# Optimization experiments

Hardware: AMD Instinct MI355X
Metric: run time of the kernel (lower is better)

Reference implementation:

```python
import jax, jax.numpy as jnp
import numpy as np

# Model config (matches init_kwargs)
L_F, DELTA_F, L_S, DELTA_S = 1, 1, 32, 16
HIDDEN = 32       # SSM state dim H
GRU_H = 64        # slow-branch GRU hidden
N_GRU = 4
B, T = 4, 32768


def setup_inputs() -> dict:
    key = jax.random.key(0)
    ks = jax.random.split(key, 13)
    def nrm(k, shape, s=0.05):
        return jax.random.normal(k, shape, dtype=jnp.float32) * s
    return {
        "x": jax.random.normal(ks[0], (B, T), dtype=jnp.float32),
        # SlowBranch params
        "fc_in_w": nrm(ks[1], (GRU_H, 1), 0.3),
        "fc_in_b": nrm(ks[2], (GRU_H,)),
        "gru_wih": nrm(ks[3], (N_GRU, 3 * GRU_H, GRU_H), 0.1),
        "gru_whh": nrm(ks[4], (N_GRU, 3 * GRU_H, GRU_H), 0.1),
        "gru_bih": nrm(ks[5], (N_GRU, 3 * GRU_H)),
        "gru_bhh": nrm(ks[6], (N_GRU, 3 * GRU_H)),
        "out_fc_w": nrm(ks[7], (2 * HIDDEN, GRU_H), 0.1),
        "out_fc_b": nrm(ks[8], (2 * HIDDEN,)),
        # Fast branch params (F_IN: 1->H, F_OUT: H->1)
        "fin_w": nrm(ks[9], (HIDDEN, 1), 0.3),
        "fin_b": nrm(ks[10], (HIDDEN,)),
        "fout_w": nrm(ks[11], (1, HIDDEN), 0.1),
        "fout_b": nrm(ks[12], (1,)),
    }


def _gru_layer(xs, Wih, Whh, bih, bhh):
    """Torch-convention GRU layer. xs: (N, L, H_in) -> (N, L, H)."""
    H = Whh.shape[1]
    # Precompute input-side gate pre-activations: (N, L, 3H)
    xp = jnp.einsum('nlh,gh->nlg', xs, Wih) + bih
    def step(h, xt):
        gh = h @ Whh.T + bhh                       # (N, 3H)
        ir, iz, inew = jnp.split(xt, 3, axis=-1)
        hr, hz, hnew = jnp.split(gh, 3, axis=-1)
        r = jax.nn.sigmoid(ir + hr)
        z = jax.nn.sigmoid(iz + hz)
        n = jnp.tanh(inew + r * hnew)
        h = (1.0 - z) * n + z * h
        return h, h
    h0 = jnp.zeros((xs.shape[0], H), xs.dtype)
    _, ys = jax.lax.scan(step, h0, jnp.swapaxes(xp, 0, 1))  # (L, N, H)
    return jnp.swapaxes(ys, 0, 1)


def reference(x, fc_in_w, fc_in_b, gru_wih, gru_whh, gru_bih, gru_bhh,
              out_fc_w, out_fc_b, fin_w, fin_b, fout_w, fout_b):
    Bsz, Tlen = x.shape
    num_slow = (Tlen - L_S) // DELTA_S + 1

    frame_idx = jnp.arange(num_slow)[:, None] * DELTA_S + jnp.arange(L_S)[None, :]
    x_s = x[:, frame_idx].reshape(Bsz * num_slow, L_S, 1)      # (N, L_s, 1)
    h = jax.nn.relu(x_s * fc_in_w[:, 0] + fc_in_b)             # (N, L_s, GRU_H)
    for l in range(gru_wih.shape[0]):
        h = _gru_layer(h, gru_wih[l], gru_whh[l], gru_bih[l], gru_bhh[l])
    eps = h[:, -1, :] @ out_fc_w.T + out_fc_b                  # (N, 2H)
    eps = eps.reshape(Bsz, num_slow, 2 * HIDDEN)
    A_slow = jax.nn.sigmoid(eps[..., :HIDDEN])                 # (B, S, H)
    g_slow = eps[..., HIDDEN:]                                 # (B, S, H)

    # ---- Fast branch: per-sample diagonal linear SSM scan ----
    delta = DELTA_S // DELTA_F
    idx = jnp.clip(jnp.arange(Tlen) // delta - 1, 0, num_slow - 1)  # (T,)
    A_t = A_slow[:, idx, :]                                    # (B, T, H)
    u_t = (x[..., None] * fin_w[:, 0] + fin_b) * g_slow[:, idx, :]  # (B, T, H)

    def step(hc, inp):
        A, u = inp
        hn = A * hc + u
        return hn, hn
    h0 = jnp.zeros((Bsz, HIDDEN), x.dtype)
    _, h_all = jax.lax.scan(step, h0,
                            (jnp.swapaxes(A_t, 0, 1), jnp.swapaxes(u_t, 0, 1)))
    # h_all: (T, B, H); F_OUT applied to every state
    return jnp.einsum('tbh,h->bt', h_all, fout_w[0]) + fout_b[0]   # (B, T)
```

## Files before the change

### kernel.cpp

```cpp
#include <hip/hip_runtime.h>
#include <hip/hip_bf16.h>

typedef __bf16 bf16x8 __attribute__((ext_vector_type(8)));
typedef short short8 __attribute__((ext_vector_type(8)));
typedef float f32x4 __attribute__((ext_vector_type(4)));
typedef unsigned short ushort_t;

#define T_LEN 32768
#define B_SZ 4
#define NSLOW 2047
#define NSEQ (B_SZ * NSLOW)
#define GH 64
#define G3 192
#define NL 4
#define HID 32
#define NCH 256
#define L2E 1.44269504088896341f

#define OFF_X    0
#define OFF_FCW  131072
#define OFF_FCB  131136
#define OFF_WIH  131200
#define OFF_WHH  180352
#define OFF_BIH  229504
#define OFF_BHH  230272
#define OFF_OFW  231040
#define OFF_OFB  235136
#define OFF_FINW 235200
#define OFF_FINB 235232
#define OFF_FOW  235264
#define OFF_FOB  235296
#define CONV_TOTAL 235297
#define CONV_PAD_BYTES 470656

static __device__ __forceinline__ float bf2f(ushort_t u) {
    union { unsigned u; float f; } c; c.u = ((unsigned)u) << 16; return c.f;
}
static __device__ __forceinline__ ushort_t f2bf(float f) {
    union { float f; unsigned u; } c; c.f = f;
    unsigned r = (c.u + 0x7FFFu + ((c.u >> 16) & 1u)) >> 16;
    return (ushort_t)r;
}
static __device__ __forceinline__ unsigned pk2bf(float a, float b) {
    float2 f; f.x = a; f.y = b;
    __hip_bfloat162 h = __float22bfloat162_rn(f);
    unsigned u;
    __builtin_memcpy(&u, &h, 4);
    return u;
}
static __device__ __forceinline__ f32x4 mfma16(short8 a, short8 b, f32x4 c) {
    return __builtin_amdgcn_mfma_f32_16x16x32_bf16(
        __builtin_bit_cast(bf16x8, a), __builtin_bit_cast(bf16x8, b), c, 0, 0, 0);
}
static __device__ __forceinline__ int xoff(int t, int kb, int seq) {
    return ((((t << 3) + kb) << 4) + (seq ^ (kb & 7))) << 3;
}
static __device__ __forceinline__ short8 load_frag_scaled(const ushort_t* p, float s) {
    uint4 r = *(const uint4*)p;
    unsigned aa[4] = {r.x, r.y, r.z, r.w};
    short8 o;
#pragma unroll
    for (int i = 0; i < 4; ++i) {
        o[2 * i]     = (short)f2bf(bf2f((ushort_t)(aa[i] & 0xffffu)) * s);
        o[2 * i + 1] = (short)f2bf(bf2f((ushort_t)(aa[i] >> 16)) * s);
    }
    return o;
}

struct Ptrs13 { const void* p[13]; };

__global__ __launch_bounds__(256) void convert_kernel(Ptrs13 ptrs,
                                                      int* __restrict__ flag,
                                                      ushort_t* __restrict__ dst)
{
    __shared__ int scnt;
    if (threadIdx.x == 0) scnt = 0;
    __syncthreads();
    {
        ushort_t u = ((const ushort_t*)ptrs.p[0])[threadIdx.x];
        int e = (u >> 7) & 0xFF;
        int ok = (e >= 80 && e <= 141) ? 1 : 0;
#pragma unroll
        for (int d = 1; d < 64; d <<= 1) ok += __shfl_xor(ok, d, 64);
        if ((threadIdx.x & 63) == 0) atomicAdd(&scnt, ok);
    }
    __syncthreads();
    const bool isbf = (scnt >= 224);
    if (blockIdx.x == 0 && threadIdx.x == 0) *flag = isbf ? 1 : 0;

    const int offs[14] = {OFF_X, OFF_FCW, OFF_FCB, OFF_WIH, OFF_WHH, OFF_BIH,
                          OFF_BHH, OFF_OFW, OFF_OFB, OFF_FINW, OFF_FINB,
                          OFF_FOW, OFF_FOB, CONV_TOTAL};
    for (int idx = blockIdx.x * 256 + threadIdx.x; idx < CONV_TOTAL;
         idx += gridDim.x * 256) {
        int s = 0;
#pragma unroll
        for (int j = 1; j < 13; ++j) if (idx >= offs[j]) s = j;
        int k = idx - offs[s];
        ushort_t v = isbf ? ((const ushort_t*)ptrs.p[s])[k]
                          : f2bf(((const float*)ptrs.p[s])[k]);
        dst[idx] = v;
    }
}

__global__ __launch_bounds__(256, 2) void gru_kernel(
    const ushort_t* __restrict__ x, const ushort_t* __restrict__ fcw,
    const ushort_t* __restrict__ fcb, const ushort_t* __restrict__ wih,
    const ushort_t* __restrict__ whh, const ushort_t* __restrict__ bih,
    const ushort_t* __restrict__ bhh, const ushort_t* __restrict__ ofw,
    const ushort_t* __restrict__ ofb, float* __restrict__ Aslow,
    float* __restrict__ gslow)
{
    __shared__ short8 Xs8[4096];
    short* Xs = (short*)Xs8;
    const int tid = threadIdx.x;
    const int w = tid >> 6, lane = tid & 63;
    const int q = lane >> 4, m = lane & 15;
    const int jb = w * 16;
    const int n0 = blockIdx.x * 16;

#pragma unroll 1
    for (int ii = 0; ii < 16; ++ii) {
        int cid = ii * 256 + tid;
        int seq = cid & 15, kb = (cid >> 4) & 7, t = cid >> 7;
        int n = n0 + seq; if (n > NSEQ - 1) n = NSEQ - 1;
        int b = n / NSLOW, s = n - b * NSLOW;
        float xv = bf2f(x[b * T_LEN + s * 16 + t]);
        short8 v;
#pragma unroll
        for (int i = 0; i < 8; ++i) {
            int g = kb * 8 + i;
            float h = fmaf(xv, bf2f(fcw[g]), bf2f(fcb[g]));
            h = h > 0.f ? h : 0.f;
            v[i] = (short)f2bf(h);
        }
        Xs8[xoff(t, kb, seq) >> 3] = v;
    }

    const int col0 = jb + 4 * q;
    const int kbw = (col0 >> 3);
    const int wsub = (col0 & 7);
    const int kofs = q * 8;
    const int wbase0 = ((kbw << 4) + (m ^ (kbw & 7))) * 8 + wsub;

    float hc[4];
#pragma unroll 1
    for (int l = 0; l < NL; ++l) {
        const ushort_t* wl = wih + l * G3 * GH;
        const ushort_t* ul = whh + l * G3 * GH;
        short8 wR0 = load_frag_scaled(wl + (0 * 64 + jb + m) * 64 + kofs, -L2E);
        short8 wR1 = load_frag_scaled(wl + (0 * 64 + jb + m) * 64 + 32 + kofs, -L2E);
        short8 wZ0 = load_frag_scaled(wl + (1 * 64 + jb + m) * 64 + kofs, -L2E);
        short8 wZ1 = load_frag_scaled(wl + (1 * 64 + jb + m) * 64 + 32 + kofs, -L2E);
        short8 wN0 = load_frag_scaled(wl + (2 * 64 + jb + m) * 64 + kofs, 2.f * L2E);
        short8 wN1 = load_frag_scaled(wl + (2 * 64 + jb + m) * 64 + 32 + kofs, 2.f * L2E);
        short8 uR0 = load_frag_scaled(ul + (0 * 64 + jb + m) * 64 + kofs, -L2E);
        short8 uR1 = load_frag_scaled(ul + (0 * 64 + jb + m) * 64 + 32 + kofs, -L2E);
        short8 uZ0 = load_frag_scaled(ul + (1 * 64 + jb + m) * 64 + kofs, -L2E);
        short8 uZ1 = load_frag_scaled(ul + (1 * 64 + jb + m) * 64 + 32 + kofs, -L2E);
        short8 uN0 = load_frag_scaled(ul + (2 * 64 + jb + m) * 64 + kofs, 2.f * L2E);
        short8 uN1 = load_frag_scaled(ul + (2 * 64 + jb + m) * 64 + 32 + kofs, 2.f * L2E);

        f32x4 bRv, bZv, bNXv, bNHv;
#pragma unroll
        for (int i = 0; i < 4; ++i) {
            int c = col0 + i;
            bRv[i]  = -L2E * (bf2f(bih[l * G3 + c]) + bf2f(bhh[l * G3 + c]));
            bZv[i]  = -L2E * (bf2f(bih[l * G3 + 64 + c]) + bf2f(bhh[l * G3 + 64 + c]));
            bNXv[i] = 2.f * L2E * bf2f(bih[l * G3 + 128 + c]);
            bNHv[i] = 2.f * L2E * bf2f(bhh[l * G3 + 128 + c]);
        }

        hc[0] = hc[1] = hc[2] = hc[3] = 0.f;

        __syncthreads();
        int iA = xoff(0, q, m) >> 3;
        int iB = xoff(0, 4 + q, m) >> 3;
        int wb = wbase0;

        short8 cx0 = Xs8[iA], cx1 = Xs8[iB];
        short8 nx0 = Xs8[iA + 128], nx1 = Xs8[iB + 128];
        f32x4 xR = bRv, xZ = bZv, xN = bNXv;
        xR = mfma16(wR0, cx0, xR); xR = mfma16(wR1, cx1, xR);
        xZ = mfma16(wZ0, cx0, xZ); xZ = mfma16(wZ1, cx1, xZ);
        xN = mfma16(wN0, cx0, xN); xN = mfma16(wN1, cx1, xN);
#pragma unroll
        for (int i = 0; i < 4; ++i) {
            float r = __builtin_amdgcn_rcpf(1.f + __builtin_amdgcn_exp2f(xR[i]));
            float z = __builtin_amdgcn_rcpf(1.f + __builtin_amdgcn_exp2f(xZ[i]));
            float yp = fmaf(r, bNHv[i], xN[i]);
            float nn = fmaf(-2.f,
                __builtin_amdgcn_rcpf(1.f + __builtin_amdgcn_exp2f(yp)), 1.f);
            hc[i] = fmaf(z, hc[i] - nn, nn);
        }
        *(uint2*)(Xs + wb) = make_uint2(pk2bf(hc[0], hc[1]), pk2bf(hc[2], hc[3]));
        xR = bRv; xZ = bZv; xN = bNXv;
        xR = mfma16(wR0, nx0, xR); xR = mfma16(wR1, nx1, xR);
        xZ = mfma16(wZ0, nx0, xZ); xZ = mfma16(wZ1, nx1, xZ);
        xN = mfma16(wN0, nx0, xN); xN = mfma16(wN1, nx1, xN);
        iA += 128; iB += 128; wb += 1024;

#pragma unroll 1
        for (int t = 1; t < 32; ++t) {
            __syncthreads();
            short8 bh0 = Xs8[iA - 128];
            short8 bh1 = Xs8[iB - 128];
            short8 px0, px1;
            if (t < 31) {
                px0 = Xs8[iA + 128];
                px1 = Xs8[iB + 128];
            }
            f32x4 aR = xR, aZ = xZ, aNH = bNHv;
            aR  = mfma16(uR0, bh0, aR);  aR  = mfma16(uR1, bh1, aR);
            aZ  = mfma16(uZ0, bh0, aZ);  aZ  = mfma16(uZ1, bh1, aZ);
            aNH = mfma16(uN0, bh0, aNH); aNH = mfma16(uN1, bh1, aNH);
#pragma unroll
            for (int i = 0; i < 4; ++i) {
                float r = __builtin_amdgcn_rcpf(1.f + __builtin_amdgcn_exp2f(aR[i]));
                float z = __builtin_amdgcn_rcpf(1.f + __builtin_amdgcn_exp2f(aZ[i]));
                float yp = fmaf(r, aNH[i], xN[i]);
                float nn = fmaf(-2.f,
                    __builtin_amdgcn_rcpf(1.f + __builtin_amdgcn_exp2f(yp)), 1.f);
                hc[i] = fmaf(z, hc[i] - nn, nn);
            }
            *(uint2*)(Xs + wb) =
                make_uint2(pk2bf(hc[0], hc[1]), pk2bf(hc[2], hc[3]));
            if (t < 31) {
                xR = bRv; xZ = bZv; xN = bNXv;
                xR = mfma16(wR0, px0, xR); xR = mfma16(wR1, px1, xR);
                xZ = mfma16(wZ0, px0, xZ); xZ = mfma16(wZ1, px1, xZ);
                xN = mfma16(wN0, px0, xN); xN = mfma16(wN1, px1, xN);
            }
            iA += 128; iB += 128; wb += 1024;
        }
    }

    __syncthreads();
    short8 aL0 = Xs8[xoff(31, q, m) >> 3];
    short8 aL1 = Xs8[xoff(31, 4 + q, m) >> 3];
    float sc = (w < 2) ? -L2E : 1.f;
    short8 o0 = load_frag_scaled(ofw + (jb + m) * 64 + kofs, sc);
    short8 o1 = load_frag_scaled(ofw + (jb + m) * 64 + 32 + kofs, sc);
    f32x4 aE = {bf2f(ofb[col0]) * sc, bf2f(ofb[col0 + 1]) * sc,
                bf2f(ofb[col0 + 2]) * sc, bf2f(ofb[col0 + 3]) * sc};
    aE = mfma16(o0, aL0, aE);
    aE = mfma16(o1, aL1, aE);
    int n = n0 + m;
    if (w < 2) {
        f32x4 v;
#pragma unroll
        for (int i = 0; i < 4; ++i)
            v[i] = __builtin_amdgcn_rcpf(1.f + __builtin_amdgcn_exp2f(aE[i]));
        *(f32x4*)(Aslow + n * HID + col0) = v;
    } else {
        *(f32x4*)(gslow + n * HID + (col0 - 32)) = aE;
    }
}

__global__ __launch_bounds__(256) void pass1_kernel(
    const ushort_t* __restrict__ x, const float* __restrict__ Aslow,
    const float* __restrict__ gslow, const ushort_t* __restrict__ finw,
    const ushort_t* __restrict__ finb, float* __restrict__ P,
    float* __restrict__ S)
{
    int gt = blockIdx.x * 256 + threadIdx.x;
    int h = gt & 31, c = (gt >> 5) & 255, b = gt >> 13;
    float fw = bf2f(finw[h]), fb = bf2f(finb[h]);
    float Pv = 1.f, Sv = 0.f;
    int t0 = c * 128;
#pragma unroll 1
    for (int seg = 0; seg < 8; ++seg) {
        int sidx = (t0 >> 4) + seg - 1;
        if (sidx < 0) sidx = 0;
        if (sidx > NSLOW - 1) sidx = NSLOW - 1;
        float A = Aslow[(b * NSLOW + sidx) * HID + h];
        float g = gslow[(b * NSLOW + sidx) * HID + h];
        float fwg = fw * g, fbg = fb * g;
        const uint4* px = (const uint4*)(x + b * T_LEN + t0 + seg * 16);
        uint4 ra = px[0], rb = px[1];
        unsigned xa[8] = {ra.x, ra.y, ra.z, ra.w, rb.x, rb.y, rb.z, rb.w};
#pragma unroll
        for (int j = 0; j < 8; ++j) {
            float x0 = bf2f((ushort_t)(xa[j] & 0xffffu));
            float x1 = bf2f((ushort_t)(xa[j] >> 16));
            Sv = fmaf(A, Sv, fmaf(x0, fwg, fbg));
            Sv = fmaf(A, Sv, fmaf(x1, fwg, fbg));
        }
        float A2 = A * A, A4 = A2 * A2, A8 = A4 * A4;
        Pv *= A8 * A8;
    }
    P[(b * HID + h) * NCH + c] = Pv;
    S[(b * HID + h) * NCH + c] = Sv;
}

__global__ __launch_bounds__(128) void scan_kernel(
    const float* __restrict__ P, const float* __restrict__ S,
    float* __restrict__ Hpre)
{
    int tid = threadIdx.x;
    const float4* p4 = (const float4*)(P + tid * NCH);
    const float4* s4 = (const float4*)(S + tid * NCH);
    float* hp = Hpre + tid * NCH;
    float hr = 0.f;
#pragma unroll 8
    for (int c = 0; c < NCH / 4; ++c) {
        float4 pv = p4[c], sv = s4[c];
        hp[4 * c + 0] = hr; hr = fmaf(pv.x, hr, sv.x);
        hp[4 * c + 1] = hr; hr = fmaf(pv.y, hr, sv.y);
        hp[4 * c + 2] = hr; hr = fmaf(pv.z, hr, sv.z);
        hp[4 * c + 3] = hr; hr = fmaf(pv.w, hr, sv.w);
    }
}

__global__ __launch_bounds__(256) void pass2_kernel(
    const ushort_t* __restrict__ x, const float* __restrict__ Aslow,
    const float* __restrict__ gslow, const float* __restrict__ Hpre,
    const ushort_t* __restrict__ finw, const ushort_t* __restrict__ finb,
    const ushort_t* __restrict__ fow, const ushort_t* __restrict__ fob,
    const int* __restrict__ flag, void* __restrict__ outv)
{
    int wv = blockIdx.x * 4 + (threadIdx.x >> 6);
    int lane = threadIdx.x & 63;
    int half = lane >> 5, h = lane & 31;
    int pair = wv * 2 + half;
    int b = pair >> 8, c = pair & 255;
    const bool isbf = (*flag != 0);
    ushort_t* outb = (ushort_t*)outv;
    float* outf = (float*)outv;
    float hv = Hpre[(b * HID + h) * NCH + c];
    float fw = bf2f(finw[h]), fb = bf2f(finb[h]);
    float wo = bf2f(fow[h]), ob = bf2f(fob[0]);
    int t0 = c * 128;
#pragma unroll 1
    for (int blk = 0; blk < 4; ++blk) {
        float ykeep = 0.f;
        float A = 0.f, fwg = 0.f, fbg = 0.f;
#pragma unroll
        for (int tt = 0; tt < 32; ++tt) {
            int t = t0 + blk * 32 + tt;
            if ((tt & 15) == 0) {
                int sidx = (t >> 4) - 1;
                if (sidx < 0) sidx = 0;
                A = Aslow[(b * NSLOW + sidx) * HID + h];
                float g = gslow[(b * NSLOW + sidx) * HID + h];
                fwg = fw * g; fbg = fb * g;
            }
            float xv = bf2f(x[b * T_LEN + t]);
            hv = fmaf(A, hv, fmaf(xv, fwg, fbg));
            float y = hv * wo;
            y += __shfl_xor(y, 1, 64);
            y += __shfl_xor(y, 2, 64);
            y += __shfl_xor(y, 4, 64);
            y += __shfl_xor(y, 8, 64);
            y += __shfl_xor(y, 16, 64);
            if (tt == h) ykeep = y + ob;
        }
        int oidx = b * T_LEN + t0 + blk * 32 + h;
        if (isbf) outb[oidx] = f2bf(ykeep);
        else      outf[oidx] = ykeep;
    }
}

extern "C" void kernel_launch(void* const* d_in, const int* in_sizes, int n_in,
                              void* d_out, int out_size, void* d_ws, size_t ws_size,
                              hipStream_t stream)
{
    ushort_t* cv = (ushort_t*)d_ws;
    const ushort_t* x    = cv + OFF_X;
    const ushort_t* fcw  = cv + OFF_FCW;
    const ushort_t* fcb  = cv + OFF_FCB;
    const ushort_t* wih  = cv + OFF_WIH;
    const ushort_t* whh  = cv + OFF_WHH;
    const ushort_t* bih  = cv + OFF_BIH;
    const ushort_t* bhh  = cv + OFF_BHH;
    const ushort_t* ofw  = cv + OFF_OFW;
    const ushort_t* ofb  = cv + OFF_OFB;
    const ushort_t* finw = cv + OFF_FINW;
    const ushort_t* finb = cv + OFF_FINB;
    const ushort_t* fow  = cv + OFF_FOW;
    const ushort_t* fob  = cv + OFF_FOB;

    float* Aslow = (float*)((char*)d_ws + CONV_PAD_BYTES);
    float* gslow = Aslow + 8192 * 32;
    float* P     = gslow + 8192 * 32;
    float* S     = P + 4 * 32 * NCH;
    float* Hpre  = S + 4 * 32 * NCH;
    int*   flag  = (int*)(Hpre + 4 * 32 * NCH);

    Ptrs13 ptrs;
    for (int i = 0; i < 13; ++i) ptrs.p[i] = d_in[i];

    convert_kernel<<<dim3(920), dim3(256), 0, stream>>>(ptrs, flag, cv);
    gru_kernel<<<dim3(512), dim3(256), 0, stream>>>(
        x, fcw, fcb, wih, whh, bih, bhh, ofw, ofb, Aslow, gslow);
    pass1_kernel<<<dim3(128), dim3(256), 0, stream>>>(
        x, Aslow, gslow, finw, finb, P, S);
    scan_kernel<<<dim3(1), dim3(128), 0, stream>>>(P, S, Hpre);
    pass2_kernel<<<dim3(128), dim3(256), 0, stream>>>(
        x, Aslow, gslow, Hpre, finw, finb, fow, fob, flag, d_out);
}
```

Baseline: 193.1 us.

## Pipeline pairs of GRU layers in a staggered wavefront over timesteps

The GRU layers now run two at a time: layer 2p+1 trails layer 2p by two timesteps, and both share the in-place LDS sequence buffer within one loop. This replaces 64 barrier-separated serial steps per layer pair with 34, and lets the independent MFMA and transcendental chains of the two layers overlap to hide recurrence latency. Per-layer weights and state move into a struct, so two full sets of weight fragments stay live at once. That roughly doubles register pressure and risks spills under the 2-blocks-per-SM launch bound. Correctness depends on the two-step skew keeping the in-place reads and writes from overlapping.

Measured after the change: 198.3 us. 2.7% more time.

```diff
diff --git a/kernel.cpp b/kernel.cpp
--- a/kernel.cpp
+++ b/kernel.cpp
@@ -103,6 +103,93 @@
     }
 }
 
+struct LayerState {
+    short8 wR0, wR1, wZ0, wZ1, wN0, wN1;
+    short8 uR0, uR1, uZ0, uZ1, uN0, uN1;
+    f32x4 bR, bZ, bNX, bNH;
+    f32x4 xR, xZ, xN;
+    f32x4 hc;
+};
+
+static __device__ __forceinline__ void load_layer(
+    LayerState& L, int l, const ushort_t* __restrict__ wih,
+    const ushort_t* __restrict__ whh, const ushort_t* __restrict__ bih,
+    const ushort_t* __restrict__ bhh, int jb, int m, int kofs, int col0)
+{
+    const ushort_t* wl = wih + l * G3 * GH;
+    const ushort_t* ul = whh + l * G3 * GH;
+    L.wR0 = load_frag_scaled(wl + (0 * 64 + jb + m) * 64 + kofs, -L2E);
+    L.wR1 = load_frag_scaled(wl + (0 * 64 + jb + m) * 64 + 32 + kofs, -L2E);
+    L.wZ0 = load_frag_scaled(wl + (1 * 64 + jb + m) * 64 + kofs, -L2E);
+    L.wZ1 = load_frag_scaled(wl + (1 * 64 + jb + m) * 64 + 32 + kofs, -L2E);
+    L.wN0 = load_frag_scaled(wl + (2 * 64 + jb + m) * 64 + kofs, 2.f * L2E);
+    L.wN1 = load_frag_scaled(wl + (2 * 64 + jb + m) * 64 + 32 + kofs, 2.f * L2E);
+    L.uR0 = load_frag_scaled(ul + (0 * 64 + jb + m) * 64 + kofs, -L2E);
+    L.uR1 = load_frag_scaled(ul + (0 * 64 + jb + m) * 64 + 32 + kofs, -L2E);
+    L.uZ0 = load_frag_scaled(ul + (1 * 64 + jb + m) * 64 + kofs, -L2E);
+    L.uZ1 = load_frag_scaled(ul + (1 * 64 + jb + m) * 64 + 32 + kofs, -L2E);
+    L.uN0 = load_frag_scaled(ul + (2 * 64 + jb + m) * 64 + kofs, 2.f * L2E);
+    L.uN1 = load_frag_scaled(ul + (2 * 64 + jb + m) * 64 + 32 + kofs, 2.f * L2E);
+#pragma unroll
+    for (int i = 0; i < 4; ++i) {
+        int c = col0 + i;
+        L.bR[i]  = -L2E * (bf2f(bih[l * G3 + c]) + bf2f(bhh[l * G3 + c]));
+        L.bZ[i]  = -L2E * (bf2f(bih[l * G3 + 64 + c]) + bf2f(bhh[l * G3 + 64 + c]));
+        L.bNX[i] = 2.f * L2E * bf2f(bih[l * G3 + 128 + c]);
+        L.bNH[i] = 2.f * L2E * bf2f(bhh[l * G3 + 128 + c]);
+    }
+    L.hc[0] = L.hc[1] = L.hc[2] = L.hc[3] = 0.f;
+}
+
+static __device__ __forceinline__ void gru_step(
+    LayerState& L, int t, short8* Xs8, short* Xs, int iA0, int iB0, int wb0)
+{
+    if (t < 0 || t > 31) return;
+    const int iA = iA0 + (t << 7);
+    const int iB = iB0 + (t << 7);
+    short8 px0, px1;
+    if (t < 31) {
+        px0 = Xs8[iA + 128];
+        px1 = Xs8[iB + 128];
+    }
+    f32x4 aR, aZ, aNH = L.bNH;
+    if (t == 0) {
+        short8 cx0 = Xs8[iA], cx1 = Xs8[iB];
+        f32x4 xR = L.bR, xZ = L.bZ, xN = L.bNX;
+        xR = mfma16(L.wR0, cx0, xR); xR = mfma16(L.wR1, cx1, xR);
+        xZ = mfma16(L.wZ0, cx0, xZ); xZ = mfma16(L.wZ1, cx1, xZ);
+        xN = mfma16(L.wN0, cx0, xN); xN = mfma16(L.wN1, cx1, xN);
+        L.xR = xR; L.xZ = xZ; L.xN = xN;
+        aR = xR; aZ = xZ;
+    } else {
+        short8 bh0 = Xs8[iA - 128];
+        short8 bh1 = Xs8[iB - 128];
+        aR  = mfma16(L.uR0, bh0, L.xR); aR  = mfma16(L.uR1, bh1, aR);
+        aZ  = mfma16(L.uZ0, bh0, L.xZ); aZ  = mfma16(L.uZ1, bh1, aZ);
+        aNH = mfma16(L.uN0, bh0, aNH);  aNH = mfma16(L.uN1, bh1, aNH);
+    }
+    f32x4 hcv = L.hc;
+#pragma unroll
+    for (int i = 0; i < 4; ++i) {
+        float r = __builtin_amdgcn_rcpf(1.f + __builtin_amdgcn_exp2f(aR[i]));
+        float z = __builtin_amdgcn_rcpf(1.f + __builtin_amdgcn_exp2f(aZ[i]));
+        float yp = fmaf(r, aNH[i], L.xN[i]);
+        float nn = fmaf(-2.f,
+            __builtin_amdgcn_rcpf(1.f + __builtin_amdgcn_exp2f(yp)), 1.f);
+        hcv[i] = fmaf(z, hcv[i] - nn, nn);
+    }
+    L.hc = hcv;
+    *(uint2*)(Xs + wb0 + (t << 10)) =
+        make_uint2(pk2bf(hcv[0], hcv[1]), pk2bf(hcv[2], hcv[3]));
+    if (t < 31) {
+        f32x4 xR = L.bR, xZ = L.bZ, xN = L.bNX;
+        xR = mfma16(L.wR0, px0, xR); xR = mfma16(L.wR1, px1, xR);
+        xZ = mfma16(L.wZ0, px0, xZ); xZ = mfma16(L.wZ1, px1, xZ);
+        xN = mfma16(L.wN0, px0, xN); xN = mfma16(L.wN1, px1, xN);
+        L.xR = xR; L.xZ = xZ; L.xN = xN;
+    }
+}
+
 __global__ __launch_bounds__(256, 2) void gru_kernel(
     const ushort_t* __restrict__ x, const ushort_t* __restrict__ fcw,
     const ushort_t* __restrict__ fcb, const ushort_t* __restrict__ wih,
@@ -142,96 +229,19 @@
     const int wsub = (col0 & 7);
     const int kofs = q * 8;
     const int wbase0 = ((kbw << 4) + (m ^ (kbw & 7))) * 8 + wsub;
-
-    float hc[4];
+    const int iA0 = xoff(0, q, m) >> 3;
+    const int iB0 = xoff(0, 4 + q, m) >> 3;
+
 #pragma unroll 1
-    for (int l = 0; l < NL; ++l) {
-        const ushort_t* wl = wih + l * G3 * GH;
-        const ushort_t* ul = whh + l * G3 * GH;
-        short8 wR0 = load_frag_scaled(wl + (0 * 64 + jb + m) * 64 + kofs, -L2E);
-        short8 wR1 = load_frag_scaled(wl + (0 * 64 + jb + m) * 64 + 32 + kofs, -L2E);
-        short8 wZ0 = load_frag_scaled(wl + (1 * 64 + jb + m) * 64 + kofs, -L2E);
-        short8 wZ1 = load_frag_scaled(wl + (1 * 64 + jb + m) * 64 + 32 + kofs, -L2E);
-        short8 wN0 = load_frag_scaled(wl + (2 * 64 + jb + m) * 64 + kofs, 2.f * L2E);
-        short8 wN1 = load_frag_scaled(wl + (2 * 64 + jb + m) * 64 + 32 + kofs, 2.f * L2E);
-        short8 uR0 = load_frag_scaled(ul + (0 * 64 + jb + m) * 64 + kofs, -L2E);
-        short8 uR1 = load_frag_scaled(ul + (0 * 64 + jb + m) * 64 + 32 + kofs, -L2E);
-        short8 uZ0 = load_frag_scaled(ul + (1 * 64 + jb + m) * 64 + kofs, -L2E);
-        short8 uZ1 = load_frag_scaled(ul + (1 * 64 + jb + m) * 64 + 32 + kofs, -L2E);
-        short8 uN0 = load_frag_scaled(ul + (2 * 64 + jb + m) * 64 + kofs, 2.f * L2E);
-        short8 uN1 = load_frag_scaled(ul + (2 * 64 + jb + m) * 64 + 32 + kofs, 2.f * L2E);
-
-        f32x4 bRv, bZv, bNXv, bNHv;
-#pragma unroll
-        for (int i = 0; i < 4; ++i) {
-            int c = col0 + i;
-            bRv[i]  = -L2E * (bf2f(bih[l * G3 + c]) + bf2f(bhh[l * G3 + c]));
-            bZv[i]  = -L2E * (bf2f(bih[l * G3 + 64 + c]) + bf2f(bhh[l * G3 + 64 + c]));
-            bNXv[i] = 2.f * L2E * bf2f(bih[l * G3 + 128 + c]);
-            bNHv[i] = 2.f * L2E * bf2f(bhh[l * G3 + 128 + c]);
-        }
-
-        hc[0] = hc[1] = hc[2] = hc[3] = 0.f;
-
-        __syncthreads();
-        int iA = xoff(0, q, m) >> 3;
-        int iB = xoff(0, 4 + q, m) >> 3;
-        int wb = wbase0;
-
-        short8 cx0 = Xs8[iA], cx1 = Xs8[iB];
-        short8 nx0 = Xs8[iA + 128], nx1 = Xs8[iB + 128];
-        f32x4 xR = bRv, xZ = bZv, xN = bNXv;
-        xR = mfma16(wR0, cx0, xR); xR = mfma16(wR1, cx1, xR);
-        xZ = mfma16(wZ0, cx0, xZ); xZ = mfma16(wZ1, cx1, xZ);
-        xN = mfma16(wN0, cx0, xN); xN = mfma16(wN1, cx1, xN);
-#pragma unroll
-        for (int i = 0; i < 4; ++i) {
-            float r = __builtin_amdgcn_rcpf(1.f + __builtin_amdgcn_exp2f(xR[i]));
-            float z = __builtin_amdgcn_rcpf(1.f + __builtin_amdgcn_exp2f(xZ[i]));
-            float yp = fmaf(r, bNHv[i], xN[i]);
-            float nn = fmaf(-2.f,
-                __builtin_amdgcn_rcpf(1.f + __builtin_amdgcn_exp2f(yp)), 1.f);
-            hc[i] = fmaf(z, hc[i] - nn, nn);
-        }
-        *(uint2*)(Xs + wb) = make_uint2(pk2bf(hc[0], hc[1]), pk2bf(hc[2], hc[3]));
-        xR = bRv; xZ = bZv; xN = bNXv;
-        xR = mfma16(wR0, nx0, xR); xR = mfma16(wR1, nx1, xR);
-        xZ = mfma16(wZ0, nx0, xZ); xZ = mfma16(wZ1, nx1, xZ);
-        xN = mfma16(wN0, nx0, xN); xN = mfma16(wN1, nx1, xN);
-        iA += 128; iB += 128; wb += 1024;
-
+    for (int p = 0; p < 2; ++p) {
+        LayerState LA, LB;
+        load_layer(LA, 2 * p,     wih, whh, bih, bhh, jb, m, kofs, col0);
+        load_layer(LB, 2 * p + 1, wih, whh, bih, bhh, jb, m, kofs, col0);
 #pragma unroll 1
-        for (int t = 1; t < 32; ++t) {
+        for (int s = 0; s < 34; ++s) {
             __syncthreads();
-            short8 bh0 = Xs8[iA - 128];
-            short8 bh1 = Xs8[iB - 128];
-            short8 px0, px1;
-            if (t < 31) {
-                px0 = Xs8[iA + 128];
-                px1 = Xs8[iB + 128];
-            }
-            f32x4 aR = xR, aZ = xZ, aNH = bNHv;
-            aR  = mfma16(uR0, bh0, aR);  aR  = mfma16(uR1, bh1, aR);
-            aZ  = mfma16(uZ0, bh0, aZ);  aZ  = mfma16(uZ1, bh1, aZ);
-            aNH = mfma16(uN0, bh0, aNH); aNH = mfma16(uN1, bh1, aNH);
-#pragma unroll
-            for (int i = 0; i < 4; ++i) {
-                float r = __builtin_amdgcn_rcpf(1.f + __builtin_amdgcn_exp2f(aR[i]));
-                float z = __builtin_amdgcn_rcpf(1.f + __builtin_amdgcn_exp2f(aZ[i]));
-                float yp = fmaf(r, aNH[i], xN[i]);
-                float nn = fmaf(-2.f,
-                    __builtin_amdgcn_rcpf(1.f + __builtin_amdgcn_exp2f(yp)), 1.f);
-                hc[i] = fmaf(z, hc[i] - nn, nn);
-            }
-            *(uint2*)(Xs + wb) =
-                make_uint2(pk2bf(hc[0], hc[1]), pk2bf(hc[2], hc[3]));
-            if (t < 31) {
-                xR = bRv; xZ = bZv; xN = bNXv;
-                xR = mfma16(wR0, px0, xR); xR = mfma16(wR1, px1, xR);
-                xZ = mfma16(wZ0, px0, xZ); xZ = mfma16(wZ1, px1, xZ);
-                xN = mfma16(wN0, px0, xN); xN = mfma16(wN1, px1, xN);
-            }
-            iA += 128; iB += 128; wb += 1024;
+            gru_step(LA, s,     Xs8, Xs, iA0, iB0, wbase0);
+            gru_step(LB, s - 2, Xs8, Xs, iA0, iB0, wbase0);
         }
     }
 
```

## Wavefront-pipeline the four GRU layers across warp groups with a shared-memory ring

Applied to the files above, without the earlier changes.

The GRU kernel grows from 256 to 1024 threads per block so that each group of four waves owns one GRU layer. The layers run as a diagonal wavefront: layer l handles timestep s-2l and hands its hidden states to the next layer through a 4-slot ring buffer in LDS. This replaces the serial layer-by-layer loop, cutting the number of barrier-separated steps per block from 128 to 38 and keeping each layer's weights resident in registers. In exchange every block needs much more LDS and many more threads, and the 1024-thread launch bound may squeeze registers and lower occupancy.

Result: slower. 203.6 us (+5.4%).

```diff
diff --git a/kernel.cpp b/kernel.cpp
--- a/kernel.cpp
+++ b/kernel.cpp
@@ -103,7 +103,7 @@
     }
 }
 
-__global__ __launch_bounds__(256, 2) void gru_kernel(
+__global__ __launch_bounds__(1024, 4) void gru_kernel(
     const ushort_t* __restrict__ x, const ushort_t* __restrict__ fcw,
     const ushort_t* __restrict__ fcb, const ushort_t* __restrict__ wih,
     const ushort_t* __restrict__ whh, const ushort_t* __restrict__ bih,
@@ -111,17 +111,19 @@
     const ushort_t* __restrict__ ofb, float* __restrict__ Aslow,
     float* __restrict__ gslow)
 {
-    __shared__ short8 Xs8[4096];
-    short* Xs = (short*)Xs8;
+    __shared__ short8 X0s[4096];
+    __shared__ short8 Rg[2048];
+    short* RgS = (short*)Rg;
     const int tid = threadIdx.x;
-    const int w = tid >> 6, lane = tid & 63;
+    const int W = tid >> 6, lane = tid & 63;
+    const int l = W >> 2, w = W & 3;
     const int q = lane >> 4, m = lane & 15;
     const int jb = w * 16;
     const int n0 = blockIdx.x * 16;
 
 #pragma unroll 1
-    for (int ii = 0; ii < 16; ++ii) {
-        int cid = ii * 256 + tid;
+    for (int ii = 0; ii < 4; ++ii) {
+        int cid = ii * 1024 + tid;
         int seq = cid & 15, kb = (cid >> 4) & 7, t = cid >> 7;
         int n = n0 + seq; if (n > NSEQ - 1) n = NSEQ - 1;
         int b = n / NSLOW, s = n - b * NSLOW;
@@ -134,7 +136,7 @@
             h = h > 0.f ? h : 0.f;
             v[i] = (short)f2bf(h);
         }
-        Xs8[xoff(t, kb, seq) >> 3] = v;
+        X0s[xoff(t, kb, seq) >> 3] = v;
     }
 
     const int col0 = jb + 4 * q;
@@ -142,118 +144,104 @@
     const int wsub = (col0 & 7);
     const int kofs = q * 8;
     const int wbase0 = ((kbw << 4) + (m ^ (kbw & 7))) * 8 + wsub;
-
-    float hc[4];
+    const int iA0 = (q << 4) + (m ^ q);
+    const int iB0 = ((4 + q) << 4) + (m ^ ((4 + q) & 7));
+
+    const ushort_t* wl = wih + l * G3 * GH;
+    const ushort_t* ul = whh + l * G3 * GH;
+    short8 wR0 = load_frag_scaled(wl + (0 * 64 + jb + m) * 64 + kofs, -L2E);
+    short8 wR1 = load_frag_scaled(wl + (0 * 64 + jb + m) * 64 + 32 + kofs, -L2E);
+    short8 wZ0 = load_frag_scaled(wl + (1 * 64 + jb + m) * 64 + kofs, -L2E);
+    short8 wZ1 = load_frag_scaled(wl + (1 * 64 + jb + m) * 64 + 32 + kofs, -L2E);
+    short8 wN0 = load_frag_scaled(wl + (2 * 64 + jb + m) * 64 + kofs, 2.f * L2E);
+    short8 wN1 = load_frag_scaled(wl + (2 * 64 + jb + m) * 64 + 32 + kofs, 2.f * L2E);
+    short8 uR0 = load_frag_scaled(ul + (0 * 64 + jb + m) * 64 + kofs, -L2E);
+    short8 uR1 = load_frag_scaled(ul + (0 * 64 + jb + m) * 64 + 32 + kofs, -L2E);
+    short8 uZ0 = load_frag_scaled(ul + (1 * 64 + jb + m) * 64 + kofs, -L2E);
+    short8 uZ1 = load_frag_scaled(ul + (1 * 64 + jb + m) * 64 + 32 + kofs, -L2E);
+    short8 uN0 = load_frag_scaled(ul + (2 * 64 + jb + m) * 64 + kofs, 2.f * L2E);
+    short8 uN1 = load_frag_scaled(ul + (2 * 64 + jb + m) * 64 + 32 + kofs, 2.f * L2E);
+
+    f32x4 bRv, bZv, bNXv, bNHv;
+#pragma unroll
+    for (int i = 0; i < 4; ++i) {
+        int c = col0 + i;
+        bRv[i]  = -L2E * (bf2f(bih[l * G3 + c]) + bf2f(bhh[l * G3 + c]));
+        bZv[i]  = -L2E * (bf2f(bih[l * G3 + 64 + c]) + bf2f(bhh[l * G3 + 64 + c]));
+        bNXv[i] = 2.f * L2E * bf2f(bih[l * G3 + 128 + c]);
+        bNHv[i] = 2.f * L2E * bf2f(bhh[l * G3 + 128 + c]);
+    }
+
+    const short8* inb = (l == 0) ? X0s : (Rg + (l - 1) * 512);
+    const short8* ringL = Rg + l * 512;
+    const int wbL = l * 4096 + wbase0;
+
+    float hc[4] = {0.f, 0.f, 0.f, 0.f};
+    f32x4 xR = {0.f, 0.f, 0.f, 0.f}, xZ = xR, xN = xR;
+
 #pragma unroll 1
-    for (int l = 0; l < NL; ++l) {
-        const ushort_t* wl = wih + l * G3 * GH;
-        const ushort_t* ul = whh + l * G3 * GH;
-        short8 wR0 = load_frag_scaled(wl + (0 * 64 + jb + m) * 64 + kofs, -L2E);
-        short8 wR1 = load_frag_scaled(wl + (0 * 64 + jb + m) * 64 + 32 + kofs, -L2E);
-        short8 wZ0 = load_frag_scaled(wl + (1 * 64 + jb + m) * 64 + kofs, -L2E);
-        short8 wZ1 = load_frag_scaled(wl + (1 * 64 + jb + m) * 64 + 32 + kofs, -L2E);
-        short8 wN0 = load_frag_scaled(wl + (2 * 64 + jb + m) * 64 + kofs, 2.f * L2E);
-        short8 wN1 = load_frag_scaled(wl + (2 * 64 + jb + m) * 64 + 32 + kofs, 2.f * L2E);
-        short8 uR0 = load_frag_scaled(ul + (0 * 64 + jb + m) * 64 + kofs, -L2E);
-        short8 uR1 = load_frag_scaled(ul + (0 * 64 + jb + m) * 64 + 32 + kofs, -L2E);
-        short8 uZ0 = load_frag_scaled(ul + (1 * 64 + jb + m) * 64 + kofs, -L2E);
-        short8 uZ1 = load_frag_scaled(ul + (1 * 64 + jb + m) * 64 + 32 + kofs, -L2E);
-        short8 uN0 = load_frag_scaled(ul + (2 * 64 + jb + m) * 64 + kofs, 2.f * L2E);
-        short8 uN1 = load_frag_scaled(ul + (2 * 64 + jb + m) * 64 + 32 + kofs, 2.f * L2E);
-
-        f32x4 bRv, bZv, bNXv, bNHv;
+    for (int s = 0; s < 38; ++s) {
+        __syncthreads();
+        int t = s - 2 * l;
+        if ((unsigned)t > 31u) continue;
+
+        f32x4 aR, aZ, aNH = bNHv;
+        if (t == 0) {
+            short8 cx0 = inb[iA0], cx1 = inb[iB0];
+            xR = bRv; xZ = bZv; xN = bNXv;
+            xR = mfma16(wR0, cx0, xR); xR = mfma16(wR1, cx1, xR);
+            xZ = mfma16(wZ0, cx0, xZ); xZ = mfma16(wZ1, cx1, xZ);
+            xN = mfma16(wN0, cx0, xN); xN = mfma16(wN1, cx1, xN);
+            aR = xR; aZ = xZ;
+        } else {
+            int si = ((t - 1) & 3) << 7;
+            short8 bh0 = ringL[si + iA0], bh1 = ringL[si + iB0];
+            aR  = mfma16(uR0, bh0, xR);  aR  = mfma16(uR1, bh1, aR);
+            aZ  = mfma16(uZ0, bh0, xZ);  aZ  = mfma16(uZ1, bh1, aZ);
+            aNH = mfma16(uN0, bh0, aNH); aNH = mfma16(uN1, bh1, aNH);
+        }
 #pragma unroll
         for (int i = 0; i < 4; ++i) {
-            int c = col0 + i;
-            bRv[i]  = -L2E * (bf2f(bih[l * G3 + c]) + bf2f(bhh[l * G3 + c]));
-            bZv[i]  = -L2E * (bf2f(bih[l * G3 + 64 + c]) + bf2f(bhh[l * G3 + 64 + c]));
-            bNXv[i] = 2.f * L2E * bf2f(bih[l * G3 + 128 + c]);
-            bNHv[i] = 2.f * L2E * bf2f(bhh[l * G3 + 128 + c]);
-        }
-
-        hc[0] = hc[1] = hc[2] = hc[3] = 0.f;
-
-        __syncthreads();
-        int iA = xoff(0, q, m) >> 3;
-        int iB = xoff(0, 4 + q, m) >> 3;
-        int wb = wbase0;
-
-        short8 cx0 = Xs8[iA], cx1 = Xs8[iB];
-        short8 nx0 = Xs8[iA + 128], nx1 = Xs8[iB + 128];
-        f32x4 xR = bRv, xZ = bZv, xN = bNXv;
-        xR = mfma16(wR0, cx0, xR); xR = mfma16(wR1, cx1, xR);
-        xZ = mfma16(wZ0, cx0, xZ); xZ = mfma16(wZ1, cx1, xZ);
-        xN = mfma16(wN0, cx0, xN); xN = mfma16(wN1, cx1, xN);
-#pragma unroll
-        for (int i = 0; i < 4; ++i) {
-            float r = __builtin_amdgcn_rcpf(1.f + __builtin_amdgcn_exp2f(xR[i]));
-            float z = __builtin_amdgcn_rcpf(1.f + __builtin_amdgcn_exp2f(xZ[i]));
-            float yp = fmaf(r, bNHv[i], xN[i]);
+            float r = __builtin_amdgcn_rcpf(1.f + __builtin_amdgcn_exp2f(aR[i]));
+            float z = __builtin_amdgcn_rcpf(1.f + __builtin_amdgcn_exp2f(aZ[i]));
+            float yp = fmaf(r, aNH[i], xN[i]);
             float nn = fmaf(-2.f,
                 __builtin_amdgcn_rcpf(1.f + __builtin_amdgcn_exp2f(yp)), 1.f);
             hc[i] = fmaf(z, hc[i] - nn, nn);
         }
-        *(uint2*)(Xs + wb) = make_uint2(pk2bf(hc[0], hc[1]), pk2bf(hc[2], hc[3]));
-        xR = bRv; xZ = bZv; xN = bNXv;
-        xR = mfma16(wR0, nx0, xR); xR = mfma16(wR1, nx1, xR);
-        xZ = mfma16(wZ0, nx0, xZ); xZ = mfma16(wZ1, nx1, xZ);
-        xN = mfma16(wN0, nx0, xN); xN = mfma16(wN1, nx1, xN);
-        iA += 128; iB += 128; wb += 1024;
-
-#pragma unroll 1
-        for (int t = 1; t < 32; ++t) {
-            __syncthreads();
-            short8 bh0 = Xs8[iA - 128];
-            short8 bh1 = Xs8[iB - 128];
-            short8 px0, px1;
-            if (t < 31) {
-                px0 = Xs8[iA + 128];
-                px1 = Xs8[iB + 128];
-            }
-            f32x4 aR = xR, aZ = xZ, aNH = bNHv;
-            aR  = mfma16(uR0, bh0, aR);  aR  = mfma16(uR1, bh1, aR);
-            aZ  = mfma16(uZ0, bh0, aZ);  aZ  = mfma16(uZ1, bh1, aZ);
-            aNH = mfma16(uN0, bh0, aNH); aNH = mfma16(uN1, bh1, aNH);
-#pragma unroll
-            for (int i = 0; i < 4; ++i) {
-                float r = __builtin_amdgcn_rcpf(1.f + __builtin_amdgcn_exp2f(aR[i]));
-                float z = __builtin_amdgcn_rcpf(1.f + __builtin_amdgcn_exp2f(aZ[i]));
-                float yp = fmaf(r, aNH[i], xN[i]);
-                float nn = fmaf(-2.f,
-                    __builtin_amdgcn_rcpf(1.f + __builtin_amdgcn_exp2f(yp)), 1.f);
-                hc[i] = fmaf(z, hc[i] - nn, nn);
-            }
-            *(uint2*)(Xs + wb) =
-                make_uint2(pk2bf(hc[0], hc[1]), pk2bf(hc[2], hc[3]));
-            if (t < 31) {
-                xR = bRv; xZ = bZv; xN = bNXv;
-                xR = mfma16(wR0, px0, xR); xR = mfma16(wR1, px1, xR);
-                xZ = mfma16(wZ0, px0, xZ); xZ = mfma16(wZ1, px1, xZ);
-                xN = mfma16(wN0, px0, xN); xN = mfma16(wN1, px1, xN);
-            }
-            iA += 128; iB += 128; wb += 1024;
+        *(uint2*)(RgS + wbL + ((t & 3) << 10)) =
+            make_uint2(pk2bf(hc[0], hc[1]), pk2bf(hc[2], hc[3]));
+        if (t < 31) {
+            int si = ((l == 0) ? (t + 1) : ((t + 1) & 3)) << 7;
+            short8 px0 = inb[si + iA0], px1 = inb[si + iB0];
+            xR = bRv; xZ = bZv; xN = bNXv;
+            xR = mfma16(wR0, px0, xR); xR = mfma16(wR1, px1, xR);
+            xZ = mfma16(wZ0, px0, xZ); xZ = mfma16(wZ1, px1, xZ);
+            xN = mfma16(wN0, px0, xN); xN = mfma16(wN1, px1, xN);
         }
     }
 
     __syncthreads();
-    short8 aL0 = Xs8[xoff(31, q, m) >> 3];
-    short8 aL1 = Xs8[xoff(31, 4 + q, m) >> 3];
-    float sc = (w < 2) ? -L2E : 1.f;
-    short8 o0 = load_frag_scaled(ofw + (jb + m) * 64 + kofs, sc);
-    short8 o1 = load_frag_scaled(ofw + (jb + m) * 64 + 32 + kofs, sc);
-    f32x4 aE = {bf2f(ofb[col0]) * sc, bf2f(ofb[col0 + 1]) * sc,
-                bf2f(ofb[col0 + 2]) * sc, bf2f(ofb[col0 + 3]) * sc};
-    aE = mfma16(o0, aL0, aE);
-    aE = mfma16(o1, aL1, aE);
-    int n = n0 + m;
-    if (w < 2) {
-        f32x4 v;
-#pragma unroll
-        for (int i = 0; i < 4; ++i)
-            v[i] = __builtin_amdgcn_rcpf(1.f + __builtin_amdgcn_exp2f(aE[i]));
-        *(f32x4*)(Aslow + n * HID + col0) = v;
-    } else {
-        *(f32x4*)(gslow + n * HID + (col0 - 32)) = aE;
+    if (l == 3) {
+        short8 aL0 = Rg[15 * 128 + iA0];
+        short8 aL1 = Rg[15 * 128 + iB0];
+        float sc = (w < 2) ? -L2E : 1.f;
+        short8 o0 = load_frag_scaled(ofw + (jb + m) * 64 + kofs, sc);
+        short8 o1 = load_frag_scaled(ofw + (jb + m) * 64 + 32 + kofs, sc);
+        f32x4 aE = {bf2f(ofb[col0]) * sc, bf2f(ofb[col0 + 1]) * sc,
+                    bf2f(ofb[col0 + 2]) * sc, bf2f(ofb[col0 + 3]) * sc};
+        aE = mfma16(o0, aL0, aE);
+        aE = mfma16(o1, aL1, aE);
+        int n = n0 + m;
+        if (w < 2) {
+            f32x4 v;
+#pragma unroll
+            for (int i = 0; i < 4; ++i)
+                v[i] = __builtin_amdgcn_rcpf(1.f + __builtin_amdgcn_exp2f(aE[i]));
+            *(f32x4*)(Aslow + n * HID + col0) = v;
+        } else {
+            *(f32x4*)(gslow + n * HID + (col0 - 32)) = aE;
+        }
     }
 }
 
@@ -391,7 +379,7 @@
     for (int i = 0; i < 13; ++i) ptrs.p[i] = d_in[i];
 
     convert_kernel<<<dim3(920), dim3(256), 0, stream>>>(ptrs, flag, cv);
-    gru_kernel<<<dim3(512), dim3(256), 0, stream>>>(
+    gru_kernel<<<dim3(512), dim3(1024), 0, stream>>>(
         x, fcw, fcb, wih, whh, bih, bhh, ofw, ofb, Aslow, gslow);
     pass1_kernel<<<dim3(128), dim3(256), 0, stream>>>(
         x, Aslow, gslow, finw, finb, P, S);
```
